# Performance work log

Measured on AMD Instinct MI355X. Metric: run time of the kernel, lower is better.

The kernel has to match this reference:

```python
import jax, jax.numpy as jnp
import numpy as np

M_DIM = 256.0  # scaling denominator from __init__ (sqrt(256) = 16)

def setup_inputs() -> dict:
    key = jax.random.key(0)
    kq, kk, kv = jax.random.split(key, 3)
    B, H, S, D = 2, 8, 4096, 64
    q = jax.random.normal(kq, (B, H, S, D), dtype=jnp.float32)
    k = jax.random.normal(kk, (B, H, S, D), dtype=jnp.float32)
    v = jax.random.normal(kv, (B, H, S, D), dtype=jnp.float32)
    return {"q": q, "k": k, "v": v}

def reference(q, k, v):
    # scores: [B, H, S, S] = q @ k^T / sqrt(m_dim)
    scores = jnp.einsum('bhqd,bhkd->bhqk', q, k) / jnp.sqrt(jnp.float32(M_DIM))
    attn = jax.nn.softmax(scores, axis=-1)
    # outputs: [B, H, S, D]
    return jnp.einsum('bhqk,bhkd->bhqd', attn, v)
```

## Files before the change

### kernel.cpp

```cpp
#include <hip/hip_runtime.h>
#include <hip/hip_bf16.h>
#include <stdint.h>

#define SEQ 4096
#define DH  64
#define KT  32
#define PS  40
#define NIT ((SEQ / 2) / KT)
#define QSCALE 0.090168440f

typedef __attribute__((ext_vector_type(8))) short short8;
typedef __attribute__((ext_vector_type(4))) float floatx4;

__device__ __forceinline__ ushort f2bf_rne(float f) {
    unsigned u = __float_as_uint(f);
    unsigned r = u + 0x7FFFu + ((u >> 16) & 1u);
    return (ushort)(r >> 16);
}

__global__ __launch_bounds__(256)
void prep_kv(const float* __restrict__ K, const float* __restrict__ V,
             ushort* __restrict__ Kf, ushort* __restrict__ Vf) {
    const int bh = blockIdx.y, kb0 = blockIdx.x * 128, t = threadIdx.x;
    const size_t inB = ((size_t)bh * SEQ + kb0) * DH;
    {
        const float* srcB = K + inB;
        ushort* dstB = Kf + (size_t)bh * SEQ * DH + (size_t)(kb0 >> 4) * 1024;
        #pragma unroll
        for (int p = 0; p < 4; ++p) {
            int c   = p * 256 + t;
            int g   = c >> 7, rem = c & 127;
            int tt  = rem >> 6, lam = rem & 63;
            int key = g * 16 + (lam & 15);
            int d0  = tt * 32 + (lam >> 4) * 8;
            const float* s = srcB + (size_t)key * DH + d0;
            float4 a = *(const float4*)s;
            float4 b = *(const float4*)(s + 4);
            short8 o;
            o[0] = (short)f2bf_rne(a.x); o[1] = (short)f2bf_rne(a.y);
            o[2] = (short)f2bf_rne(a.z); o[3] = (short)f2bf_rne(a.w);
            o[4] = (short)f2bf_rne(b.x); o[5] = (short)f2bf_rne(b.y);
            o[6] = (short)f2bf_rne(b.z); o[7] = (short)f2bf_rne(b.w);
            *(short8*)(dstB + g * 1024 + tt * 512 + lam * 8) = o;
        }
    }
    {
        const int d0 = (t & 15) * 4, sl = (t >> 4) * 8;
        const float* src = V + inB + (size_t)sl * DH + d0;
        ushort* dstB = Vf + (size_t)bh * SEQ * DH + (size_t)(kb0 >> 5) * 2048;
        ushort b[8][4];
        #pragma unroll
        for (int r = 0; r < 8; ++r) {
            float4 f = *(const float4*)(src + r * DH);
            b[r][0] = f2bf_rne(f.x); b[r][1] = f2bf_rne(f.y);
            b[r][2] = f2bf_rne(f.z); b[r][3] = f2bf_rne(f.w);
        }
        const int Tl = sl >> 5, kq = (sl & 31) >> 3;
        #pragma unroll
        for (int i = 0; i < 4; ++i) {
            int d = d0 + i;
            short8 w;
            #pragma unroll
            for (int r = 0; r < 8; ++r) w[r] = (short)b[r][i];
            *(short8*)(dstB + Tl * 2048 + (d >> 4) * 512 + kq * 128 + (d & 15) * 8) = w;
        }
    }
}

__global__ __launch_bounds__(256, 4)
void attn_fwd_v7(const float* __restrict__ Q, const ushort* __restrict__ Kf,
                 const ushort* __restrict__ Vf, float* __restrict__ O)
{
    __shared__ __align__(16) char smem[17664];

    const int g    = blockIdx.x;
    const int bh   = (g & 7) * 2 + ((g >> 3) & 1);
    const int qt0  = (g >> 4) * 64;

    const int tid   = threadIdx.x;
    const int wave  = tid >> 6;
    const int widx  = wave & 1;
    const int wpair = wave >> 1;
    const int lane  = tid & 63;
    const int n16   = lane & 15;
    const int quad  = lane >> 4;

    const float* Qb  = Q + ((size_t)bh * SEQ) * DH;
    const char*  KfB = (const char*)(Kf + (size_t)bh * SEQ * DH);
    const char*  VfB = (const char*)(Vf + (size_t)bh * SEQ * DH);
    float*       Ob  = O + ((size_t)bh * SEQ) * DH;

    ushort* sPw = (ushort*)smem + wave * (32 * PS);

    const int qw0 = qt0 + widx * 32;
    short8 qfrag[2][2];
    #pragma unroll
    for (int qt = 0; qt < 2; ++qt) {
        const float* qrow = Qb + (size_t)(qw0 + qt * 16 + n16) * DH;
        #pragma unroll
        for (int t = 0; t < 2; ++t) {
            const float* p = qrow + t * 32 + quad * 8;
            short8 a;
            #pragma unroll
            for (int j = 0; j < 8; ++j) a[j] = (short)f2bf_rne(p[j] * QSCALE);
            qfrag[qt][t] = a;
        }
    }
    short8 ones;
    #pragma unroll
    for (int j = 0; j < 8; ++j) ones[j] = (short)0x3F80;

    floatx4 oacc[2][4];
    floatx4 lacc[2];
    #pragma unroll
    for (int qt = 0; qt < 2; ++qt) {
        lacc[qt] = (floatx4){0.f, 0.f, 0.f, 0.f};
        #pragma unroll
        for (int nt = 0; nt < 4; ++nt) oacc[qt][nt] = (floatx4){0.f, 0.f, 0.f, 0.f};
    }

    const char* kp0 = KfB + (size_t)wpair * 262144 + lane * 16;
    const char* vp0 = VfB + (size_t)wpair * 262144 + lane * 16;
    const char* kp = kp0;
    const char* vp = vp0;

    short8 kf[4], vf[4];
    #pragma unroll
    for (int c = 0; c < 4; ++c) kf[c] = *(const short8*)(kp + c * 1024);
    #pragma unroll
    for (int c = 0; c < 4; ++c) vf[c] = *(const short8*)(vp + c * 1024);

    for (int it = 0; it < NIT; ++it) {
        const char* kpn = (it + 1 < NIT) ? kp + 4096 : kp0;
        const char* vpn = (it + 1 < NIT) ? vp + 4096 : vp0;

        floatx4 sacc[2][2];
        #pragma unroll
        for (int kt = 0; kt < 2; ++kt) {
            #pragma unroll
            for (int qt = 0; qt < 2; ++qt) {
                floatx4 acc = (floatx4){0.f, 0.f, 0.f, 0.f};
                acc = __builtin_amdgcn_mfma_f32_16x16x32_bf16(kf[kt * 2 + 0], qfrag[qt][0], acc, 0, 0, 0);
                acc = __builtin_amdgcn_mfma_f32_16x16x32_bf16(kf[kt * 2 + 1], qfrag[qt][1], acc, 0, 0, 0);
                sacc[kt][qt] = acc;
            }
        }
        #pragma unroll
        for (int c = 0; c < 4; ++c) kf[c] = *(const short8*)(kpn + c * 1024);

        #pragma unroll
        for (int kt = 0; kt < 2; ++kt) {
            #pragma unroll
            for (int qt = 0; qt < 2; ++qt) {
                unsigned u0 = __float_as_uint(__builtin_amdgcn_exp2f(sacc[kt][qt][0]));
                unsigned u1 = __float_as_uint(__builtin_amdgcn_exp2f(sacc[kt][qt][1]));
                unsigned u2 = __float_as_uint(__builtin_amdgcn_exp2f(sacc[kt][qt][2]));
                unsigned u3 = __float_as_uint(__builtin_amdgcn_exp2f(sacc[kt][qt][3]));
                uint2 w;
                w.x = __builtin_amdgcn_perm(u1, u0, 0x07060302);
                w.y = __builtin_amdgcn_perm(u3, u2, 0x07060302);
                *(uint2*)&sPw[(qt * 16 + n16) * PS + kt * 16 + quad * 4] = w;
            }
        }

        short8 pf[2];
        #pragma unroll
        for (int qt = 0; qt < 2; ++qt)
            pf[qt] = *(const short8*)&sPw[(qt * 16 + n16) * PS + quad * 8];

        #pragma unroll
        for (int nt = 0; nt < 4; ++nt) {
            short8 v = vf[nt];
            #pragma unroll
            for (int qt = 0; qt < 2; ++qt)
                oacc[qt][nt] = __builtin_amdgcn_mfma_f32_16x16x32_bf16(v, pf[qt], oacc[qt][nt], 0, 0, 0);
        }
        #pragma unroll
        for (int qt = 0; qt < 2; ++qt)
            lacc[qt] = __builtin_amdgcn_mfma_f32_16x16x32_bf16(ones, pf[qt], lacc[qt], 0, 0, 0);

        #pragma unroll
        for (int c = 0; c < 4; ++c) vf[c] = *(const short8*)(vpn + c * 1024);

        kp = kpn; vp = vpn;
    }

    __syncthreads();
    float* epiO = (float*)smem;
    float* epiL = (float*)(smem + 17408);
    if (wpair == 1) {
        #pragma unroll
        for (int qt = 0; qt < 2; ++qt) {
            const int row = widx * 32 + qt * 16 + n16;
            #pragma unroll
            for (int nt = 0; nt < 4; ++nt)
                *(float4*)&epiO[row * 68 + nt * 16 + quad * 4] = (float4){
                    oacc[qt][nt][0], oacc[qt][nt][1], oacc[qt][nt][2], oacc[qt][nt][3]};
            if (quad == 0) epiL[row] = lacc[qt][0];
        }
    }
    __syncthreads();
    if (wpair == 0) {
        #pragma unroll
        for (int qt = 0; qt < 2; ++qt) {
            const int row = widx * 32 + qt * 16 + n16;
            const float inv = 1.0f / (lacc[qt][0] + epiL[row]);
            const int q = qw0 + qt * 16 + n16;
            #pragma unroll
            for (int nt = 0; nt < 4; ++nt) {
                float4 part = *(const float4*)&epiO[row * 68 + nt * 16 + quad * 4];
                float4 o;
                o.x = (oacc[qt][nt][0] + part.x) * inv;
                o.y = (oacc[qt][nt][1] + part.y) * inv;
                o.z = (oacc[qt][nt][2] + part.z) * inv;
                o.w = (oacc[qt][nt][3] + part.w) * inv;
                *(float4*)&Ob[(size_t)q * DH + nt * 16 + quad * 4] = o;
            }
        }
    }
}

__global__ __launch_bounds__(256, 4)
void attn_fwd_v1(const float* __restrict__ Q, const float* __restrict__ K,
                 const float* __restrict__ V, float* __restrict__ O)
{
    __shared__ __align__(16) ushort sKf[64 * 72];
    __shared__ __align__(16) ushort sVf[64 * 72];
    __shared__ __align__(16) ushort sPf[4 * 16 * 72];
    const int bh = blockIdx.y, qt0 = blockIdx.x * 64, tid = threadIdx.x;
    const int wave = tid >> 6, lane = tid & 63, n16 = lane & 15, quad = lane >> 4;
    const size_t base = (size_t)bh * SEQ * DH;
    const float *Qb = Q + base, *Kb = K + base, *Vb = V + base;
    float* Ob = O + base;
    short8 qfrag[2];
    {
        const float* qrow = Qb + (size_t)(qt0 + wave * 16 + n16) * DH;
        #pragma unroll
        for (int t = 0; t < 2; ++t) {
            const float* p = qrow + t * 32 + quad * 8;
            short8 a;
            #pragma unroll
            for (int j = 0; j < 8; ++j) a[j] = (short)f2bf_rne(p[j] * 0.0625f);
            qfrag[t] = a;
        }
    }
    floatx4 oacc[4];
    #pragma unroll
    for (int nt = 0; nt < 4; ++nt) oacc[nt] = (floatx4){0.f,0.f,0.f,0.f};
    float m_i[4] = {-INFINITY,-INFINITY,-INFINITY,-INFINITY};
    float l_i[4] = {0.f,0.f,0.f,0.f};
    const int skr = tid >> 2, sc0 = (tid & 3) * 16;
    for (int kt0 = 0; kt0 < SEQ; kt0 += 64) {
        __syncthreads();
        const float* ksrc = Kb + (size_t)(kt0 + skr) * DH + sc0;
        const float* vsrc = Vb + (size_t)(kt0 + skr) * DH + sc0;
        ushort* kdst = &sKf[skr * 72 + sc0];
        #pragma unroll
        for (int i = 0; i < 16; i += 4) {
            float4 kf = *(const float4*)(ksrc + i);
            kdst[i+0]=f2bf_rne(kf.x); kdst[i+1]=f2bf_rne(kf.y);
            kdst[i+2]=f2bf_rne(kf.z); kdst[i+3]=f2bf_rne(kf.w);
            float4 vf = *(const float4*)(vsrc + i);
            sVf[(sc0+i+0)*72+skr]=f2bf_rne(vf.x); sVf[(sc0+i+1)*72+skr]=f2bf_rne(vf.y);
            sVf[(sc0+i+2)*72+skr]=f2bf_rne(vf.z); sVf[(sc0+i+3)*72+skr]=f2bf_rne(vf.w);
        }
        __syncthreads();
        floatx4 sacc[4];
        #pragma unroll
        for (int nt = 0; nt < 4; ++nt) {
            sacc[nt] = (floatx4){0.f,0.f,0.f,0.f};
            #pragma unroll
            for (int t = 0; t < 2; ++t) {
                short8 b = *(const short8*)&sKf[(nt*16+n16)*72 + t*32 + quad*8];
                sacc[nt] = __builtin_amdgcn_mfma_f32_16x16x32_bf16(qfrag[t], b, sacc[nt], 0,0,0);
            }
        }
        ushort* pw = &sPf[wave * 16 * 72];
        #pragma unroll
        for (int r = 0; r < 4; ++r) {
            float mx = fmaxf(fmaxf(sacc[0][r],sacc[1][r]),fmaxf(sacc[2][r],sacc[3][r]));
            #pragma unroll
            for (int off = 1; off < 16; off <<= 1) mx = fmaxf(mx, __shfl_xor(mx, off, 64));
            float mnew = fmaxf(m_i[r], mx);
            float alpha = __expf(m_i[r] - mnew);
            m_i[r] = mnew;
            float sum = 0.f;
            #pragma unroll
            for (int nt = 0; nt < 4; ++nt) {
                float p = __expf(sacc[nt][r] - mnew);
                sacc[nt][r] = p; sum += p;
            }
            #pragma unroll
            for (int off = 1; off < 16; off <<= 1) sum += __shfl_xor(sum, off, 64);
            l_i[r] = l_i[r] * alpha + sum;
            #pragma unroll
            for (int nt = 0; nt < 4; ++nt) oacc[nt][r] *= alpha;
            #pragma unroll
            for (int nt = 0; nt < 4; ++nt)
                pw[(quad*4+r)*72 + nt*16 + n16] = f2bf_rne(sacc[nt][r]);
        }
        #pragma unroll
        for (int t = 0; t < 2; ++t) {
            short8 pfr = *(const short8*)&pw[n16*72 + t*32 + quad*8];
            #pragma unroll
            for (int nt = 0; nt < 4; ++nt) {
                short8 vfr = *(const short8*)&sVf[(nt*16+n16)*72 + t*32 + quad*8];
                oacc[nt] = __builtin_amdgcn_mfma_f32_16x16x32_bf16(pfr, vfr, oacc[nt], 0,0,0);
            }
        }
    }
    #pragma unroll
    for (int r = 0; r < 4; ++r) {
        float inv = 1.0f / l_i[r];
        float* orow = Ob + (size_t)(qt0 + wave*16 + quad*4 + r) * DH;
        #pragma unroll
        for (int nt = 0; nt < 4; ++nt) orow[nt*16+n16] = oacc[nt][r] * inv;
    }
}

extern "C" void kernel_launch(void* const* d_in, const int* in_sizes, int n_in,
                              void* d_out, int out_size, void* d_ws, size_t ws_size,
                              hipStream_t stream) {
    const float* q = (const float*)d_in[0];
    const float* k = (const float*)d_in[1];
    const float* v = (const float*)d_in[2];
    float* o = (float*)d_out;
    const size_t elems = (size_t)16 * SEQ * DH;
    const size_t need  = elems * 2 * 2;
    if (ws_size >= need) {
        ushort* kf = (ushort*)d_ws;
        ushort* vf = kf + elems;
        prep_kv<<<dim3(SEQ / 128, 16), dim3(256), 0, stream>>>(k, v, kf, vf);
        attn_fwd_v7<<<dim3(1024), dim3(256), 0, stream>>>(q, kf, vf, o);
    } else {
        attn_fwd_v1<<<dim3(SEQ / 64, 16), dim3(256), 0, stream>>>(q, k, v, o);
    }
}
```

Before: 168.6 us.

## Software-pipeline attention loop with double-buffered P tile in LDS

Restructures the main loop so the PV MFMAs for step i run alongside the QK^T MFMAs and exp2 for step i+1. The P tile is double-buffered in LDS, with a prologue and epilogue added around the loop. The aim is to break the serial dependency between exp, the LDS round-trip and the PV matmul within one iteration. In exchange it grows the shared-memory footprint and register live ranges, which could hurt occupancy.

```diff
diff --git a/kernel.cpp b/kernel.cpp
--- a/kernel.cpp
+++ b/kernel.cpp
@@ -68,10 +68,10 @@
 }
 
 __global__ __launch_bounds__(256, 4)
-void attn_fwd_v7(const float* __restrict__ Q, const ushort* __restrict__ Kf,
+void attn_fwd_v8(const float* __restrict__ Q, const ushort* __restrict__ Kf,
                  const ushort* __restrict__ Vf, float* __restrict__ O)
 {
-    __shared__ __align__(16) char smem[17664];
+    __shared__ __align__(16) char smem[20480];
 
     const int g    = blockIdx.x;
     const int bh   = (g & 7) * 2 + ((g >> 3) & 1);
@@ -90,7 +90,7 @@
     const char*  VfB = (const char*)(Vf + (size_t)bh * SEQ * DH);
     float*       Ob  = O + ((size_t)bh * SEQ) * DH;
 
-    ushort* sPw = (ushort*)smem + wave * (32 * PS);
+    ushort* sPw = (ushort*)smem + wave * 2560;
 
     const int qw0 = qt0 + widx * 32;
     short8 qfrag[2][2];
@@ -121,22 +121,17 @@
 
     const char* kp0 = KfB + (size_t)wpair * 262144 + lane * 16;
     const char* vp0 = VfB + (size_t)wpair * 262144 + lane * 16;
-    const char* kp = kp0;
-    const char* vp = vp0;
 
     short8 kf[4], vf[4];
     #pragma unroll
-    for (int c = 0; c < 4; ++c) kf[c] = *(const short8*)(kp + c * 1024);
-    #pragma unroll
-    for (int c = 0; c < 4; ++c) vf[c] = *(const short8*)(vp + c * 1024);
-
-    for (int it = 0; it < NIT; ++it) {
-        const char* kpn = (it + 1 < NIT) ? kp + 4096 : kp0;
-        const char* vpn = (it + 1 < NIT) ? vp + 4096 : vp0;
-
+    for (int c = 0; c < 4; ++c) kf[c] = *(const short8*)(kp0 + c * 1024);
+    #pragma unroll
+    for (int c = 0; c < 4; ++c) vf[c] = *(const short8*)(vp0 + c * 1024);
+
+    {
         floatx4 sacc[2][2];
         #pragma unroll
-        for (int kt = 0; kt < 2; ++kt) {
+        for (int kt = 0; kt < 2; ++kt)
             #pragma unroll
             for (int qt = 0; qt < 2; ++qt) {
                 floatx4 acc = (floatx4){0.f, 0.f, 0.f, 0.f};
@@ -144,12 +139,10 @@
                 acc = __builtin_amdgcn_mfma_f32_16x16x32_bf16(kf[kt * 2 + 1], qfrag[qt][1], acc, 0, 0, 0);
                 sacc[kt][qt] = acc;
             }
-        }
-        #pragma unroll
-        for (int c = 0; c < 4; ++c) kf[c] = *(const short8*)(kpn + c * 1024);
-
-        #pragma unroll
-        for (int kt = 0; kt < 2; ++kt) {
+        #pragma unroll
+        for (int c = 0; c < 4; ++c) kf[c] = *(const short8*)(kp0 + 4096 + c * 1024);
+        #pragma unroll
+        for (int kt = 0; kt < 2; ++kt)
             #pragma unroll
             for (int qt = 0; qt < 2; ++qt) {
                 unsigned u0 = __float_as_uint(__builtin_amdgcn_exp2f(sacc[kt][qt][0]));
@@ -161,28 +154,73 @@
                 w.y = __builtin_amdgcn_perm(u3, u2, 0x07060302);
                 *(uint2*)&sPw[(qt * 16 + n16) * PS + kt * 16 + quad * 4] = w;
             }
-        }
-
-        short8 pf[2];
-        #pragma unroll
-        for (int qt = 0; qt < 2; ++qt)
-            pf[qt] = *(const short8*)&sPw[(qt * 16 + n16) * PS + quad * 8];
+    }
+
+    const char* kp = kp0 + 4096;
+    const char* vp = vp0;
+
+    for (int it = 0; it < NIT - 1; ++it) {
+        const ushort* pb = sPw + (it & 1) * 1280;
+        short8 pf0 = *(const short8*)&pb[(0 * 16 + n16) * PS + quad * 8];
+        short8 pf1 = *(const short8*)&pb[(1 * 16 + n16) * PS + quad * 8];
+
+        floatx4 sacc[2][2];
+        #pragma unroll
+        for (int kt = 0; kt < 2; ++kt)
+            #pragma unroll
+            for (int qt = 0; qt < 2; ++qt) {
+                floatx4 acc = (floatx4){0.f, 0.f, 0.f, 0.f};
+                acc = __builtin_amdgcn_mfma_f32_16x16x32_bf16(kf[kt * 2 + 0], qfrag[qt][0], acc, 0, 0, 0);
+                acc = __builtin_amdgcn_mfma_f32_16x16x32_bf16(kf[kt * 2 + 1], qfrag[qt][1], acc, 0, 0, 0);
+                sacc[kt][qt] = acc;
+            }
+
+        const char* kpn = (it + 2 < NIT) ? kp + 4096 : kp;
+        #pragma unroll
+        for (int c = 0; c < 4; ++c) kf[c] = *(const short8*)(kpn + c * 1024);
+        kp = kpn;
+
+        ushort* wb = sPw + ((it + 1) & 1) * 1280;
+        #pragma unroll
+        for (int kt = 0; kt < 2; ++kt)
+            #pragma unroll
+            for (int qt = 0; qt < 2; ++qt) {
+                unsigned u0 = __float_as_uint(__builtin_amdgcn_exp2f(sacc[kt][qt][0]));
+                unsigned u1 = __float_as_uint(__builtin_amdgcn_exp2f(sacc[kt][qt][1]));
+                unsigned u2 = __float_as_uint(__builtin_amdgcn_exp2f(sacc[kt][qt][2]));
+                unsigned u3 = __float_as_uint(__builtin_amdgcn_exp2f(sacc[kt][qt][3]));
+                uint2 w;
+                w.x = __builtin_amdgcn_perm(u1, u0, 0x07060302);
+                w.y = __builtin_amdgcn_perm(u3, u2, 0x07060302);
+                *(uint2*)&wb[(qt * 16 + n16) * PS + kt * 16 + quad * 4] = w;
+            }
 
         #pragma unroll
         for (int nt = 0; nt < 4; ++nt) {
             short8 v = vf[nt];
-            #pragma unroll
-            for (int qt = 0; qt < 2; ++qt)
-                oacc[qt][nt] = __builtin_amdgcn_mfma_f32_16x16x32_bf16(v, pf[qt], oacc[qt][nt], 0, 0, 0);
-        }
-        #pragma unroll
-        for (int qt = 0; qt < 2; ++qt)
-            lacc[qt] = __builtin_amdgcn_mfma_f32_16x16x32_bf16(ones, pf[qt], lacc[qt], 0, 0, 0);
-
-        #pragma unroll
-        for (int c = 0; c < 4; ++c) vf[c] = *(const short8*)(vpn + c * 1024);
-
-        kp = kpn; vp = vpn;
+            oacc[0][nt] = __builtin_amdgcn_mfma_f32_16x16x32_bf16(v, pf0, oacc[0][nt], 0, 0, 0);
+            oacc[1][nt] = __builtin_amdgcn_mfma_f32_16x16x32_bf16(v, pf1, oacc[1][nt], 0, 0, 0);
+        }
+        lacc[0] = __builtin_amdgcn_mfma_f32_16x16x32_bf16(ones, pf0, lacc[0], 0, 0, 0);
+        lacc[1] = __builtin_amdgcn_mfma_f32_16x16x32_bf16(ones, pf1, lacc[1], 0, 0, 0);
+
+        vp += 4096;
+        #pragma unroll
+        for (int c = 0; c < 4; ++c) vf[c] = *(const short8*)(vp + c * 1024);
+    }
+
+    {
+        const ushort* pb = sPw + ((NIT - 1) & 1) * 1280;
+        short8 pf0 = *(const short8*)&pb[(0 * 16 + n16) * PS + quad * 8];
+        short8 pf1 = *(const short8*)&pb[(1 * 16 + n16) * PS + quad * 8];
+        #pragma unroll
+        for (int nt = 0; nt < 4; ++nt) {
+            short8 v = vf[nt];
+            oacc[0][nt] = __builtin_amdgcn_mfma_f32_16x16x32_bf16(v, pf0, oacc[0][nt], 0, 0, 0);
+            oacc[1][nt] = __builtin_amdgcn_mfma_f32_16x16x32_bf16(v, pf1, oacc[1][nt], 0, 0, 0);
+        }
+        lacc[0] = __builtin_amdgcn_mfma_f32_16x16x32_bf16(ones, pf0, lacc[0], 0, 0, 0);
+        lacc[1] = __builtin_amdgcn_mfma_f32_16x16x32_bf16(ones, pf1, lacc[1], 0, 0, 0);
     }
 
     __syncthreads();
@@ -331,7 +369,7 @@
         ushort* kf = (ushort*)d_ws;
         ushort* vf = kf + elems;
         prep_kv<<<dim3(SEQ / 128, 16), dim3(256), 0, stream>>>(k, v, kf, vf);
-        attn_fwd_v7<<<dim3(1024), dim3(256), 0, stream>>>(q, kf, vf, o);
+        attn_fwd_v8<<<dim3(1024), dim3(256), 0, stream>>>(q, kf, vf, o);
     } else {
         attn_fwd_v1<<<dim3(SEQ / 64, 16), dim3(256), 0, stream>>>(q, k, v, o);
     }
```

Measured after the change: 170.8 us. Within noise of the previous version (+1.3%).
